# Kernel tuning notes

Measured on AMD Instinct MI355X. Metric: run time of the kernel, lower is better.

## Reference

```python
import jax, jax.numpy as jnp
import numpy as np

B, S, DIM = 2, 2048, 2048
NH, NKV = 16, 8
HD = DIM // NH  # 128
ROPE_THETA = 10000.0


def setup_inputs() -> dict:
    key = jax.random.key(0)
    ks = jax.random.split(key, 7)
    std = DIM ** -0.5
    x = jax.random.normal(ks[0], (B, S, DIM), jnp.float32)
    wq = jax.random.normal(ks[1], (NH * HD, DIM), jnp.float32) * std
    wk = jax.random.normal(ks[2], (NKV * HD, DIM), jnp.float32) * std
    wv = jax.random.normal(ks[3], (NKV * HD, DIM), jnp.float32) * std
    wo = jax.random.normal(ks[4], (DIM, NH * HD), jnp.float32) * std
    inv_freq = 1.0 / (ROPE_THETA ** (jnp.arange(0, HD, 2, dtype=jnp.float32) / HD))
    ang = jnp.arange(S, dtype=jnp.float32)[:, None] * inv_freq[None, :]  # [S, HD//2]
    freqs_cos = jnp.cos(ang)
    freqs_sin = jnp.sin(ang)
    # diffusion-style random per-batch token mask: t ~ U[0,1) per batch row
    t = jax.random.uniform(ks[5], (B, 1))
    mask = jax.random.uniform(ks[6], (B, S)) < t  # True = masked key
    mask = mask.at[:, 0].set(False)  # first token never masked
    return dict(x=x, wq=wq, wk=wk, wv=wv, wo=wo,
                freqs_cos=freqs_cos, freqs_sin=freqs_sin, mask=mask)


def _rope(x, cos, sin):
    # x: [b, s, h, d]; pairs (x[2i], x[2i+1]) rotated by angle[s, i]
    xr, xi = x[..., 0::2], x[..., 1::2]
    c = cos[None, :, None, :]
    s = sin[None, :, None, :]
    out = jnp.stack([xr * c - xi * s, xr * s + xi * c], axis=-1)
    return out.reshape(x.shape)


def reference(x, wq, wk, wv, wo, freqs_cos, freqs_sin, mask):
    b, s, _ = x.shape
    xq = jnp.einsum('bsd,ed->bse', x, wq).reshape(b, s, NH, HD)
    xk = jnp.einsum('bsd,ed->bse', x, wk).reshape(b, s, NKV, HD)
    xv = jnp.einsum('bsd,ed->bse', x, wv).reshape(b, s, NKV, HD)
    xq = _rope(xq, freqs_cos, freqs_sin)
    xk = _rope(xk, freqs_cos, freqs_sin)
    n_rep = NH // NKV
    xk = jnp.repeat(xk, n_rep, axis=2)  # repeat_kv (GQA)
    xv = jnp.repeat(xv, n_rep, axis=2)
    q = xq.transpose(0, 2, 1, 3)  # [b, h, s, d]
    k = xk.transpose(0, 2, 1, 3)
    v = xv.transpose(0, 2, 1, 3)
    scale = 1.0 / np.sqrt(HD).astype(np.float32)
    scores = jnp.einsum('bhqd,bhkd->bhqk', q, k) * scale  # [b, h, s, s]
    scores = jnp.where(mask[:, None, None, :], -jnp.inf, scores)
    probs = jax.nn.softmax(scores, axis=-1)
    out = jnp.einsum('bhqk,bhkd->bhqd', probs, v)
    out = out.transpose(0, 2, 1, 3).reshape(b, s, NH * HD)
    return jnp.einsum('bse,de->bsd', out, wo)
```

## Files before the change

kernel.cpp:

```cpp
#include <hip/hip_runtime.h>
#include <hip/hip_bf16.h>
#include <cstdint>
#include <cstddef>

#define S_LEN   2048
#define NHQ     16
#define NKV_H   8
#define HD_DIM  128
#define DMODEL  2048
#define BATCH   2
#define KVD     (NKV_H * HD_DIM)
#define QKV_LD  4096

typedef float f32x4  __attribute__((ext_vector_type(4)));
typedef __bf16 bf16x8 __attribute__((ext_vector_type(8)));
typedef __bf16 bf16x4 __attribute__((ext_vector_type(4)));
typedef short  s16x4  __attribute__((ext_vector_type(4)));

__device__ __forceinline__ void gload_lds16(const __bf16* g, __bf16* l) {
    __builtin_amdgcn_global_load_lds(
        (const __attribute__((address_space(1))) void*)g,
        (__attribute__((address_space(3))) void*)l, 16, 0, 0);
}

__global__ __launch_bounds__(256)
void prep_kernel(const unsigned* __restrict__ x, int* __restrict__ flag_x,
                 const unsigned* __restrict__ fc, int* __restrict__ flag_fc,
                 const unsigned char* __restrict__ mraw,
                 unsigned char* __restrict__ mout, int n) {
    if (blockIdx.x == 0) {
        __shared__ int cnt;
        if (threadIdx.x == 0) cnt = 0;
        __syncthreads();
        int c = 0;
        for (int j = threadIdx.x; j < 1024; j += 256) {
            unsigned hw = x[j] & 0xFFFFu;
            unsigned e  = (hw >> 7) & 0xFF;
            if (hw == 0u || (e >= 118 && e <= 132)) c++;
        }
        atomicAdd(&cnt, c);
        __syncthreads();
        if (threadIdx.x == 0) *flag_x = (cnt > 512) ? 1 : 0;
    } else if (blockIdx.x == 1) {
        if (threadIdx.x == 0) *flag_fc = (fc[0] == 0x3F803F80u) ? 1 : 0;
    } else {
        __shared__ int f_bf16, f_f32, f_u8;
        if (threadIdx.x == 0) { f_bf16 = 0; f_f32 = 0; f_u8 = 0; }
        __syncthreads();
        const unsigned* dw = (const unsigned*)mraw;
        int ndw = n / 4;
        for (int j = threadIdx.x; j < ndw; j += blockDim.x) {
            unsigned v = dw[j];
            if (v == 0x00003F80u || v == 0x3F803F80u) f_bf16 = 1;
            else if (v == 0x3F800000u) f_f32 = 1;
            else if (v & 0xFFFFFFFEu) f_u8 = 1;
        }
        __syncthreads();
        int layout;
        if (f_bf16) layout = 3;
        else if (f_f32) layout = 2;
        else if (f_u8) layout = 0;
        else layout = 1;
        for (int i = threadIdx.x; i < n; i += blockDim.x) {
            unsigned v;
            if (layout == 0)      v = mraw[i];
            else if (layout == 3) v = ((const unsigned short*)mraw)[i];
            else                  v = ((const unsigned*)mraw)[i];
            mout[i] = v ? 1u : 0u;
        }
    }
}

__device__ __forceinline__ void conv8(const void* src, __bf16* dst,
                                      size_t off, int isbf16) {
    if (isbf16) {
        *reinterpret_cast<uint4*>(dst + off) =
            *reinterpret_cast<const uint4*>((const __bf16*)src + off);
    } else {
        const float* f = (const float*)src + off;
        float4 a = *reinterpret_cast<const float4*>(f);
        float4 b = *reinterpret_cast<const float4*>(f + 4);
        bf16x8 v;
        v[0] = (__bf16)a.x; v[1] = (__bf16)a.y; v[2] = (__bf16)a.z; v[3] = (__bf16)a.w;
        v[4] = (__bf16)b.x; v[5] = (__bf16)b.y; v[6] = (__bf16)b.z; v[7] = (__bf16)b.w;
        *reinterpret_cast<bf16x8*>(dst + off) = v;
    }
}

__global__ __launch_bounds__(256)
void conv_all_kernel(const void* __restrict__ x,  const void* __restrict__ wq,
                     const void* __restrict__ wk, const void* __restrict__ wv,
                     __bf16* __restrict__ xb, __bf16* __restrict__ wcomb,
                     const int* __restrict__ dflag) {
    int i = blockIdx.x * 256 + threadIdx.x;
    int isb = *dflag;
    if (i < 1048576) {
        conv8(x, xb, (size_t)i * 8, isb);
    } else if (i < 1572864) {
        conv8(wq, wcomb, (size_t)(i - 1048576) * 8, isb);
    } else if (i < 1835008) {
        conv8(wk, wcomb + (size_t)2048 * 2048, (size_t)(i - 1572864) * 8, isb);
    } else {
        conv8(wv, wcomb + (size_t)3072 * 2048, (size_t)(i - 1835008) * 8, isb);
    }
}

__global__ __launch_bounds__(256)
void conv_bf16_strided_kernel(const void* __restrict__ src,
                              __bf16* __restrict__ dstbase,
                              int n8, const int* __restrict__ dflag) {
    int i = blockIdx.x * blockDim.x + threadIdx.x;
    if (i >= n8) return;
    size_t off = (size_t)i * 8;
    size_t row = off >> 11;
    size_t col = off & 2047;
    __bf16* dst = dstbase + row * QKV_LD + col;
    if (*dflag) {
        *reinterpret_cast<uint4*>(dst) =
            *reinterpret_cast<const uint4*>((const __bf16*)src + off);
    } else {
        const float* f = (const float*)src + off;
        float4 a = *reinterpret_cast<const float4*>(f);
        float4 b = *reinterpret_cast<const float4*>(f + 4);
        bf16x8 v;
        v[0] = (__bf16)a.x; v[1] = (__bf16)a.y; v[2] = (__bf16)a.z; v[3] = (__bf16)a.w;
        v[4] = (__bf16)b.x; v[5] = (__bf16)b.y; v[6] = (__bf16)b.z; v[7] = (__bf16)b.w;
        *reinterpret_cast<bf16x8*>(dst) = v;
    }
}

template <bool OUT_BF16>
__global__ __launch_bounds__(256)
void gemm_bt_async(const __bf16* __restrict__ A, const __bf16* __restrict__ Bw,
                   void* __restrict__ Cv, int K, int lda, int ldb, int ldc) {
    __shared__ __align__(16) __bf16 As[128 * 64];
    __shared__ __align__(16) __bf16 Bs[128 * 64];

    const int t    = threadIdx.x;
    const int w    = t >> 6;
    const int lane = t & 63;
    const int quad = lane >> 4;
    const int l16  = lane & 15;
    const int wm   = (w >> 1) * 64;
    const int wn   = (w & 1) * 64;

    const int nwg  = gridDim.x * gridDim.y;
    const int lin  = blockIdx.y * gridDim.x + blockIdx.x;
    const int swz  = (lin & 7) * (nwg >> 3) + (lin >> 3);
    const int m0   = (swz % gridDim.x) * 128;
    const int n0   = (swz / gridDim.x) * 128;

    const int rl   = lane >> 3;
    const int gl   = lane & 7;

    f32x4 acc[4][4];
#pragma unroll
    for (int i = 0; i < 4; ++i)
#pragma unroll
        for (int j = 0; j < 4; ++j) acc[i][j] = (f32x4){0.f, 0.f, 0.f, 0.f};

    for (int k0 = 0; k0 < K; k0 += 64) {
        __syncthreads();
#pragma unroll
        for (int p = 0; p < 4; ++p) {
            const int rowb = w * 32 + p * 8;
            const int r    = rowb + rl;
            const int gA   = gl ^ rl;
            gload_lds16(A  + (size_t)(m0 + r) * lda + k0 + gA * 8, &As[rowb * 64]);
            gload_lds16(Bw + (size_t)(n0 + r) * ldb + k0 + gA * 8, &Bs[rowb * 64]);
        }
        __syncthreads();
#pragma unroll
        for (int ks = 0; ks < 2; ++ks) {
            const int G = ks * 4 + quad;
            const int gsw = (G ^ (l16 & 7)) * 8;
            bf16x8 af[4], bf[4];
#pragma unroll
            for (int i = 0; i < 4; ++i)
                af[i] = *reinterpret_cast<const bf16x8*>(
                    &As[(wm + i * 16 + l16) * 64 + gsw]);
#pragma unroll
            for (int j = 0; j < 4; ++j)
                bf[j] = *reinterpret_cast<const bf16x8*>(
                    &Bs[(wn + j * 16 + l16) * 64 + gsw]);
#pragma unroll
            for (int i = 0; i < 4; ++i)
#pragma unroll
                for (int j = 0; j < 4; ++j)
                    acc[i][j] = __builtin_amdgcn_mfma_f32_16x16x32_bf16(
                        af[i], bf[j], acc[i][j], 0, 0, 0);
        }
    }
#pragma unroll
    for (int i = 0; i < 4; ++i)
#pragma unroll
        for (int r = 0; r < 4; ++r) {
            size_t m = (size_t)(m0 + wm + i * 16 + quad * 4 + r);
#pragma unroll
            for (int j = 0; j < 4; ++j) {
                int n = n0 + wn + j * 16 + l16;
                if constexpr (OUT_BF16)
                    ((__hip_bfloat16*)Cv)[m * ldc + n] = __float2bfloat16(acc[i][j][r]);
                else
                    ((float*)Cv)[m * ldc + n] = acc[i][j][r];
            }
        }
}

__global__ void rope_kernel(__hip_bfloat16* __restrict__ xqk,
                            const void* __restrict__ cosv,
                            const void* __restrict__ sinv,
                            const int* __restrict__ dflag_fc,
                            int npairs) {
    int idx = blockIdx.x * blockDim.x + threadIdx.x;
    if (idx >= npairs) return;
    int i  = idx & 63;
    int h  = (idx >> 6) % 24;
    int bs = idx / (64 * 24);
    int s  = bs & (S_LEN - 1);
    float c, sn;
    if (*dflag_fc) {
        c  = __bfloat162float(((const __hip_bfloat16*)cosv)[s * 64 + i]);
        sn = __bfloat162float(((const __hip_bfloat16*)sinv)[s * 64 + i]);
    } else {
        c  = ((const float*)cosv)[s * 64 + i];
        sn = ((const float*)sinv)[s * 64 + i];
    }
    unsigned* p = (unsigned*)(xqk + (size_t)bs * QKV_LD + h * HD_DIM) + i;
    unsigned u = *p;
    float xr = __uint_as_float(u << 16);
    float xi = __uint_as_float(u & 0xFFFF0000u);
    float o0 = xr * c - xi * sn;
    float o1 = xr * sn + xi * c;
    union { __hip_bfloat16 h2[2]; unsigned u32; } out;
    out.h2[0] = __float2bfloat16(o0);
    out.h2[1] = __float2bfloat16(o1);
    *p = out.u32;
}

__global__ __launch_bounds__(256)
void transpose_v_kernel(const __hip_bfloat16* __restrict__ xv,
                        __hip_bfloat16* __restrict__ vt) {
    __shared__ unsigned short T[32][36];
    const int t  = threadIdx.x;
    const int s0 = blockIdx.x * 32;
    const int d0 = blockIdx.y * 32;
    const int z  = blockIdx.z;
    const int b  = z >> 3;
    const int kv = z & 7;
    {
        int sr = t >> 3, dc = (t & 7) * 4;
        const unsigned short* p = (const unsigned short*)xv
            + (size_t)(b * S_LEN + s0 + sr) * QKV_LD + kv * 128 + d0 + dc;
        uint2 v = *reinterpret_cast<const uint2*>(p);
        T[sr][dc + 0] = (unsigned short)(v.x & 0xFFFFu);
        T[sr][dc + 1] = (unsigned short)(v.x >> 16);
        T[sr][dc + 2] = (unsigned short)(v.y & 0xFFFFu);
        T[sr][dc + 3] = (unsigned short)(v.y >> 16);
    }
    __syncthreads();
    {
        int dr = t >> 3, sc = (t & 7) * 4;
        unsigned w0 = (unsigned)T[sc + 0][dr] | ((unsigned)T[sc + 1][dr] << 16);
        unsigned w1 = (unsigned)T[sc + 2][dr] | ((unsigned)T[sc + 3][dr] << 16);
        unsigned short* q = (unsigned short*)vt
            + ((size_t)z * 128 + d0 + dr) * S_LEN + s0 + sc;
        uint2 v; v.x = w0; v.y = w1;
        *reinterpret_cast<uint2*>(q) = v;
    }
}

__global__ __launch_bounds__(256)
void attn_mfma2_kernel(__hip_bfloat16* qkv,
                       const __hip_bfloat16* __restrict__ vt_g,
                       const unsigned char* __restrict__ msk) {
    __shared__ __align__(16) __bf16 Ks[2][64 * 128];
    __shared__ __align__(16) __bf16 Vt[2][128 * 64];

    const int t    = threadIdx.x;
    const int w    = t >> 6;
    const int lane = t & 63;
    const int quad = lane >> 4;
    const int l16  = lane & 15;

    const int bid = ((blockIdx.x & 7) << 7) | (blockIdx.x >> 3);
    const int qt  = bid & 31;
    const int h   = (bid >> 5) & (NHQ - 1);
    const int b   = bid >> 9;
    const int kvh = h >> 1;
    const int q0  = qt * 64;

    bf16x8 qf[4];
    {
        const __bf16* qrow = (const __bf16*)qkv
            + (size_t)(b * S_LEN + q0 + w * 16 + l16) * QKV_LD + h * 128 + quad * 8;
#pragma unroll
        for (int ks = 0; ks < 4; ++ks)
            qf[ks] = *reinterpret_cast<const bf16x8*>(qrow + ks * 32);
    }

    float m_r = -INFINITY, l_r = 0.f;
    f32x4 o[8];
#pragma unroll
    for (int d0 = 0; d0 < 8; ++d0) o[d0] = (f32x4){0.f, 0.f, 0.f, 0.f};

    const float scale2 = 0.08838834764831845f * 1.4426950408889634f;
    const int gbase = lane & 48;

    const __bf16* kp[4];
    const __bf16* vp[4];
    {
        const __bf16* xk = (const __bf16*)qkv + 2048;
        const int krl = lane >> 4, kgl = lane & 15;
        const int vrl = lane >> 3, vgl = lane & 7;
#pragma unroll
        for (int p = 0; p < 4; ++p) {
            const int row = w * 16 + p * 4 + krl;
            kp[p] = xk + (size_t)(b * S_LEN + row) * QKV_LD
                       + kvh * 128 + (kgl ^ (row & 7)) * 8;
        }
#pragma unroll
        for (int p = 0; p < 4; ++p) {
            const int row = w * 32 + p * 8 + vrl;
            vp[p] = (const __bf16*)vt_g
                  + ((size_t)(b * NKV_H + kvh) * 128 + row) * S_LEN
                  + (vgl ^ (row & 7)) * 8;
        }
    }
    const unsigned char* mbase = msk + b * S_LEN;

    auto stage = [&](int sb) {
#pragma unroll
        for (int p = 0; p < 4; ++p) {
            gload_lds16(kp[p], &Ks[sb][(w * 16 + p * 4) * 128]);
            kp[p] += 64 * QKV_LD;
        }
#pragma unroll
        for (int p = 0; p < 4; ++p) {
            gload_lds16(vp[p], &Vt[sb][(w * 32 + p * 8) * 64]);
            vp[p] += 64;
        }
    };

    auto tile_body = [&](int kmask, int cb, int sb, bool do_stage) {
        if (do_stage) stage(sb);

        unsigned mk4[4];
        {
            const unsigned* mp = (const unsigned*)(mbase + kmask);
#pragma unroll
            for (int n0 = 0; n0 < 4; ++n0) mk4[n0] = mp[n0 * 4 + quad];
        }

        f32x4 sc4[4];
#pragma unroll
        for (int n0 = 0; n0 < 4; ++n0) sc4[n0] = (f32x4){0.f, 0.f, 0.f, 0.f};
        __builtin_amdgcn_s_setprio(1);
#pragma unroll
        for (int ks = 0; ks < 4; ++ks) {
            const int G = ks * 4 + quad;
#pragma unroll
            for (int n0 = 0; n0 < 4; ++n0) {
                const int row  = n0 * 16 + l16;
                const int slot = G ^ (row & 7);
                bf16x8 kf = *reinterpret_cast<const bf16x8*>(&Ks[cb][row * 128 + slot * 8]);
                sc4[n0] = __builtin_amdgcn_mfma_f32_16x16x32_bf16(kf, qf[ks], sc4[n0], 0, 0, 0);
            }
        }
        __builtin_amdgcn_s_setprio(0);

#pragma unroll
        for (int n0 = 0; n0 < 4; ++n0)
#pragma unroll
            for (int r = 0; r < 4; ++r)
                sc4[n0][r] = ((mk4[n0] >> (r * 8)) & 0xFF) ? -INFINITY : sc4[n0][r];

        float tq[4];
#pragma unroll
        for (int n0 = 0; n0 < 4; ++n0)
            tq[n0] = fmaxf(fmaxf(sc4[n0][0], sc4[n0][1]),
                           fmaxf(sc4[n0][2], sc4[n0][3]));
        float rm = fmaxf(fmaxf(tq[0], tq[1]), fmaxf(tq[2], tq[3]));
        rm = fmaxf(rm, __shfl_xor(rm, 16, 64));
        rm = fmaxf(rm, __shfl_xor(rm, 32, 64));

        bool need = (rm - m_r) * scale2 > 8.0f;
        if (__any((int)need)) {
            float mn = fmaxf(m_r, rm);
            float al = exp2f((m_r - mn) * scale2);
            m_r = mn;
            l_r *= al;
            float alq[4];
#pragma unroll
            for (int r = 0; r < 4; ++r)
                alq[r] = __shfl(al, gbase | (quad * 4 + r), 64);
#pragma unroll
            for (int d0 = 0; d0 < 8; ++d0)
#pragma unroll
                for (int r = 0; r < 4; ++r) o[d0][r] *= alq[r];
        }

        s16x4 pa[4];
        float negm = -m_r * scale2;
#pragma unroll
        for (int n0 = 0; n0 < 4; ++n0) {
            bf16x4 pk;
#pragma unroll
            for (int r = 0; r < 4; ++r) {
                float p = exp2f(fmaf(sc4[n0][r], scale2, negm));
                l_r += p;
                pk[r] = (__bf16)p;
            }
            pa[n0] = *reinterpret_cast<s16x4*>(&pk);
        }

        __builtin_amdgcn_s_setprio(1);
#pragma unroll
        for (int n0 = 0; n0 < 4; ++n0) {
            const int j    = n0 * 16 + quad * 4;
            const int gran = j >> 3;
            const int hb   = (j & 7) * 2;
#pragma unroll
            for (int d0 = 0; d0 < 8; ++d0) {
                const int row  = d0 * 16 + l16;
                const int slot = gran ^ (row & 7);
                s16x4 vb = *reinterpret_cast<const s16x4*>(
                    (const char*)(&Vt[cb][row * 64]) + slot * 16 + hb);
                o[d0] = __builtin_amdgcn_mfma_f32_16x16x16bf16_1k(
                    pa[n0], vb, o[d0], 0, 0, 0);
            }
        }
        __builtin_amdgcn_s_setprio(0);

        __syncthreads();
    };

    stage(0);
    __syncthreads();

    for (int k0 = 0; k0 < S_LEN; k0 += 128) {
        tile_body(k0,      0, 1, true);
        tile_body(k0 + 64, 1, 0, k0 + 128 < S_LEN);
    }

    float ls = l_r;
    ls += __shfl_xor(ls, 16, 64);
    ls += __shfl_xor(ls, 32, 64);
    float invl = 1.f / ls;
    float invq[4];
#pragma unroll
    for (int r = 0; r < 4; ++r)
        invq[r] = __shfl(invl, gbase | (quad * 4 + r), 64);
    __hip_bfloat16* att = qkv;
#pragma unroll
    for (int d0 = 0; d0 < 8; ++d0)
#pragma unroll
        for (int r = 0; r < 4; ++r) {
            size_t row = (size_t)(b * S_LEN + q0 + w * 16 + quad * 4 + r);
            att[row * QKV_LD + h * 128 + d0 * 16 + l16] =
                __float2bfloat16(o[d0][r] * invq[r]);
        }
}

extern "C" void kernel_launch(void* const* d_in, const int* in_sizes, int n_in,
                              void* d_out, int out_size, void* d_ws, size_t ws_size,
                              hipStream_t stream) {
    const void* x  = d_in[0];
    const void* wq = d_in[1];
    const void* wk = d_in[2];
    const void* wv = d_in[3];
    const void* wo = d_in[4];
    const void* fc = d_in[5];
    const void* fs = d_in[6];
    const unsigned char* mraw = (const unsigned char*)d_in[7];

    const int M = BATCH * S_LEN;
    char* wsb = (char*)d_ws;
    int* dflag_x  = (int*)wsb;
    int* dflag_fc = (int*)(wsb + 64);
    unsigned char* mnorm = (unsigned char*)(wsb + 128);
    __hip_bfloat16* qkv = (__hip_bfloat16*)(wsb + 8192);

    char* dob = (char*)d_out;
    __bf16* xb    = (__bf16*)dob;
    __bf16* wcomb = (__bf16*)(dob + (16u << 20));
    __hip_bfloat16* vt = (__hip_bfloat16*)d_out;

    hipLaunchKernelGGL(prep_kernel, dim3(3), dim3(256), 0, stream,
                       (const unsigned*)x, dflag_x, (const unsigned*)fc, dflag_fc,
                       mraw, mnorm, BATCH * S_LEN);

    hipLaunchKernelGGL(conv_all_kernel, dim3(8192), dim3(256), 0, stream,
                       x, wq, wk, wv, xb, wcomb, dflag_x);

    hipLaunchKernelGGL((gemm_bt_async<true>), dim3(M / 128, QKV_LD / 128), dim3(256), 0, stream,
                       xb, wcomb, (void*)qkv, DMODEL, DMODEL, DMODEL, QKV_LD);

    int npairs = M * 24 * (HD_DIM / 2);
    hipLaunchKernelGGL(rope_kernel, dim3(npairs / 256), dim3(256), 0, stream,
                       qkv, fc, fs, dflag_fc, npairs);

    hipLaunchKernelGGL(transpose_v_kernel, dim3(S_LEN / 32, HD_DIM / 32, BATCH * NKV_H),
                       dim3(256), 0, stream, qkv + 3072, vt);

    hipLaunchKernelGGL(attn_mfma2_kernel, dim3(BATCH * NHQ * (S_LEN / 64)), dim3(256), 0, stream,
                       qkv, vt, mnorm);

    hipLaunchKernelGGL(conv_bf16_strided_kernel, dim3((DMODEL * DMODEL / 8) / 256), dim3(256), 0, stream,
                       wo, (__bf16*)qkv + 2048, DMODEL * DMODEL / 8, dflag_x);

    hipLaunchKernelGGL((gemm_bt_async<false>), dim3(M / 128, DMODEL / 128), dim3(256), 0, stream,
                       (const __bf16*)qkv, (const __bf16*)qkv + 2048, d_out,
                       DMODEL, QKV_LD, QKV_LD, DMODEL);
}
```

Before: 441.4 us.

## Software-pipeline attention: overlap next tile QK^T with current softmax/PV

Restructures the attention main loop so K and V tiles are staged at different times: the QK^T MFMA for tile i+1 is issued before the softmax and PV for tile i, keeping the matrix cores busy while exp and reduction run. P is also written to a per-wave LDS buffer and reread as bf16x8 so PV uses the 16x16x32 MFMA instead of 16x16x16. This adds LDS traffic for P and raises register pressure from two live score sets, which could lower occupancy.

```diff
diff --git a/kernel.cpp b/kernel.cpp
--- a/kernel.cpp
+++ b/kernel.cpp
@@ -15,7 +15,6 @@
 typedef float f32x4  __attribute__((ext_vector_type(4)));
 typedef __bf16 bf16x8 __attribute__((ext_vector_type(8)));
 typedef __bf16 bf16x4 __attribute__((ext_vector_type(4)));
-typedef short  s16x4  __attribute__((ext_vector_type(4)));
 
 __device__ __forceinline__ void gload_lds16(const __bf16* g, __bf16* l) {
     __builtin_amdgcn_global_load_lds(
@@ -276,6 +275,7 @@
                        const unsigned char* __restrict__ msk) {
     __shared__ __align__(16) __bf16 Ks[2][64 * 128];
     __shared__ __align__(16) __bf16 Vt[2][128 * 64];
+    __shared__ __align__(16) __bf16 Ps[4][16][64];
 
     const int t    = threadIdx.x;
     const int w    = t >> 6;
@@ -329,119 +329,116 @@
     }
     const unsigned char* mbase = msk + b * S_LEN;
 
-    auto stage = [&](int sb) {
-#pragma unroll
-        for (int p = 0; p < 4; ++p) {
-            gload_lds16(kp[p], &Ks[sb][(w * 16 + p * 4) * 128]);
-            kp[p] += 64 * QKV_LD;
-        }
-#pragma unroll
-        for (int p = 0; p < 4; ++p) {
-            gload_lds16(vp[p], &Vt[sb][(w * 32 + p * 8) * 64]);
-            vp[p] += 64;
-        }
-    };
-
-    auto tile_body = [&](int kmask, int cb, int sb, bool do_stage) {
-        if (do_stage) stage(sb);
-
-        unsigned mk4[4];
-        {
-            const unsigned* mp = (const unsigned*)(mbase + kmask);
-#pragma unroll
-            for (int n0 = 0; n0 < 4; ++n0) mk4[n0] = mp[n0 * 4 + quad];
-        }
-
-        f32x4 sc4[4];
-#pragma unroll
-        for (int n0 = 0; n0 < 4; ++n0) sc4[n0] = (f32x4){0.f, 0.f, 0.f, 0.f};
-        __builtin_amdgcn_s_setprio(1);
-#pragma unroll
-        for (int ks = 0; ks < 4; ++ks) {
-            const int G = ks * 4 + quad;
-#pragma unroll
-            for (int n0 = 0; n0 < 4; ++n0) {
-                const int row  = n0 * 16 + l16;
-                const int slot = G ^ (row & 7);
-                bf16x8 kf = *reinterpret_cast<const bf16x8*>(&Ks[cb][row * 128 + slot * 8]);
-                sc4[n0] = __builtin_amdgcn_mfma_f32_16x16x32_bf16(kf, qf[ks], sc4[n0], 0, 0, 0);
-            }
-        }
-        __builtin_amdgcn_s_setprio(0);
-
-#pragma unroll
-        for (int n0 = 0; n0 < 4; ++n0)
-#pragma unroll
-            for (int r = 0; r < 4; ++r)
-                sc4[n0][r] = ((mk4[n0] >> (r * 8)) & 0xFF) ? -INFINITY : sc4[n0][r];
-
-        float tq[4];
-#pragma unroll
-        for (int n0 = 0; n0 < 4; ++n0)
-            tq[n0] = fmaxf(fmaxf(sc4[n0][0], sc4[n0][1]),
-                           fmaxf(sc4[n0][2], sc4[n0][3]));
-        float rm = fmaxf(fmaxf(tq[0], tq[1]), fmaxf(tq[2], tq[3]));
-        rm = fmaxf(rm, __shfl_xor(rm, 16, 64));
-        rm = fmaxf(rm, __shfl_xor(rm, 32, 64));
-
-        bool need = (rm - m_r) * scale2 > 8.0f;
-        if (__any((int)need)) {
-            float mn = fmaxf(m_r, rm);
-            float al = exp2f((m_r - mn) * scale2);
-            m_r = mn;
-            l_r *= al;
-            float alq[4];
-#pragma unroll
-            for (int r = 0; r < 4; ++r)
-                alq[r] = __shfl(al, gbase | (quad * 4 + r), 64);
-#pragma unroll
-            for (int d0 = 0; d0 < 8; ++d0)
-#pragma unroll
-                for (int r = 0; r < 4; ++r) o[d0][r] *= alq[r];
-        }
-
-        s16x4 pa[4];
-        float negm = -m_r * scale2;
-#pragma unroll
-        for (int n0 = 0; n0 < 4; ++n0) {
-            bf16x4 pk;
-#pragma unroll
-            for (int r = 0; r < 4; ++r) {
-                float p = exp2f(fmaf(sc4[n0][r], scale2, negm));
-                l_r += p;
-                pk[r] = (__bf16)p;
-            }
-            pa[n0] = *reinterpret_cast<s16x4*>(&pk);
-        }
-
-        __builtin_amdgcn_s_setprio(1);
-#pragma unroll
-        for (int n0 = 0; n0 < 4; ++n0) {
-            const int j    = n0 * 16 + quad * 4;
-            const int gran = j >> 3;
-            const int hb   = (j & 7) * 2;
-#pragma unroll
-            for (int d0 = 0; d0 < 8; ++d0) {
-                const int row  = d0 * 16 + l16;
-                const int slot = gran ^ (row & 7);
-                s16x4 vb = *reinterpret_cast<const s16x4*>(
-                    (const char*)(&Vt[cb][row * 64]) + slot * 16 + hb);
-                o[d0] = __builtin_amdgcn_mfma_f32_16x16x16bf16_1k(
-                    pa[n0], vb, o[d0], 0, 0, 0);
-            }
-        }
-        __builtin_amdgcn_s_setprio(0);
-
-        __syncthreads();
-    };
-
-    stage(0);
+    f32x4 scA[4], scB[4];
+    unsigned mkA[4], mkB[4];
+
+#define STAGE_K(SB) { _Pragma("unroll") \
+    for (int p_ = 0; p_ < 4; ++p_) { \
+        gload_lds16(kp[p_], &Ks[SB][(w * 16 + p_ * 4) * 128]); \
+        kp[p_] += 64 * QKV_LD; } }
+
+#define STAGE_V(SB) { _Pragma("unroll") \
+    for (int p_ = 0; p_ < 4; ++p_) { \
+        gload_lds16(vp[p_], &Vt[SB][(w * 32 + p_ * 8) * 64]); \
+        vp[p_] += 64; } }
+
+#define LOAD_MK(MK, K0) { \
+    const unsigned* mp_ = (const unsigned*)(mbase + (K0)); \
+    _Pragma("unroll") for (int n_ = 0; n_ < 4; ++n_) MK[n_] = mp_[n_ * 4 + quad]; }
+
+#define QKT(CB, SC) { \
+    _Pragma("unroll") for (int n_ = 0; n_ < 4; ++n_) SC[n_] = (f32x4){0.f, 0.f, 0.f, 0.f}; \
+    _Pragma("unroll") for (int ks_ = 0; ks_ < 4; ++ks_) { \
+        const int G_ = ks_ * 4 + quad; \
+        _Pragma("unroll") for (int n_ = 0; n_ < 4; ++n_) { \
+            const int row_  = n_ * 16 + l16; \
+            const int slot_ = G_ ^ (row_ & 7); \
+            bf16x8 kf_ = *reinterpret_cast<const bf16x8*>(&Ks[CB][row_ * 128 + slot_ * 8]); \
+            SC[n_] = __builtin_amdgcn_mfma_f32_16x16x32_bf16(kf_, qf[ks_], SC[n_], 0, 0, 0); } } }
+
+#define SMPV(SC, MK, CB) { \
+    _Pragma("unroll") for (int n_ = 0; n_ < 4; ++n_) \
+        _Pragma("unroll") for (int r_ = 0; r_ < 4; ++r_) \
+            SC[n_][r_] = ((MK[n_] >> (r_ * 8)) & 0xFF) ? -INFINITY : SC[n_][r_]; \
+    float tq_[4]; \
+    _Pragma("unroll") for (int n_ = 0; n_ < 4; ++n_) \
+        tq_[n_] = fmaxf(fmaxf(SC[n_][0], SC[n_][1]), fmaxf(SC[n_][2], SC[n_][3])); \
+    float rm_ = fmaxf(fmaxf(tq_[0], tq_[1]), fmaxf(tq_[2], tq_[3])); \
+    rm_ = fmaxf(rm_, __shfl_xor(rm_, 16, 64)); \
+    rm_ = fmaxf(rm_, __shfl_xor(rm_, 32, 64)); \
+    bool need_ = (rm_ - m_r) * scale2 > 8.0f; \
+    if (__any((int)need_)) { \
+        float mn_ = fmaxf(m_r, rm_); \
+        float al_ = exp2f((m_r - mn_) * scale2); \
+        m_r = mn_; l_r *= al_; \
+        float alq_[4]; \
+        _Pragma("unroll") for (int r_ = 0; r_ < 4; ++r_) \
+            alq_[r_] = __shfl(al_, gbase | (quad * 4 + r_), 64); \
+        _Pragma("unroll") for (int d_ = 0; d_ < 8; ++d_) \
+            _Pragma("unroll") for (int r_ = 0; r_ < 4; ++r_) o[d_][r_] *= alq_[r_]; } \
+    float negm_ = -m_r * scale2; \
+    _Pragma("unroll") for (int n_ = 0; n_ < 4; ++n_) { \
+        _Pragma("unroll") for (int r_ = 0; r_ < 4; ++r_) { \
+            float p_ = exp2f(fmaf(SC[n_][r_], scale2, negm_)); \
+            SC[n_][r_] = p_; l_r += p_; } \
+        const int kb_    = n_ * 16 + quad * 4; \
+        const int gran_  = kb_ >> 3; \
+        const int half4_ = kb_ & 4; \
+        const int slot_  = gran_ ^ (l16 & 7); \
+        bf16x4 pk_; \
+        pk_[0] = (__bf16)SC[n_][0]; pk_[1] = (__bf16)SC[n_][1]; \
+        pk_[2] = (__bf16)SC[n_][2]; pk_[3] = (__bf16)SC[n_][3]; \
+        *reinterpret_cast<bf16x4*>(&Ps[w][l16][slot_ * 8 + half4_]) = pk_; } \
+    __builtin_amdgcn_s_setprio(1); \
+    _Pragma("unroll") for (int kk_ = 0; kk_ < 64; kk_ += 32) { \
+        const int Gp_    = (kk_ >> 3) + quad; \
+        const int slotp_ = Gp_ ^ (l16 & 7); \
+        bf16x8 af_ = *reinterpret_cast<const bf16x8*>(&Ps[w][l16][slotp_ * 8]); \
+        _Pragma("unroll") for (int d_ = 0; d_ < 8; ++d_) { \
+            const int row_  = d_ * 16 + l16; \
+            const int slot_ = Gp_ ^ (row_ & 7); \
+            bf16x8 bf_ = *reinterpret_cast<const bf16x8*>(&Vt[CB][row_ * 64 + slot_ * 8]); \
+            o[d_] = __builtin_amdgcn_mfma_f32_16x16x32_bf16(af_, bf_, o[d_], 0, 0, 0); } } \
+    __builtin_amdgcn_s_setprio(0); }
+
+    STAGE_K(0);
     __syncthreads();
 
-    for (int k0 = 0; k0 < S_LEN; k0 += 128) {
-        tile_body(k0,      0, 1, true);
-        tile_body(k0 + 64, 1, 0, k0 + 128 < S_LEN);
-    }
+    STAGE_K(1);
+    STAGE_V(0);
+    LOAD_MK(mkA, 0);
+    QKT(0, scA);
+    __syncthreads();
+
+    for (int it = 0; it < 15; ++it) {
+        const int k0 = it * 128 + 64;
+        STAGE_K(0);
+        STAGE_V(1);
+        LOAD_MK(mkB, k0);
+        QKT(1, scB);
+        SMPV(scA, mkA, 0);
+        __syncthreads();
+        STAGE_K(1);
+        STAGE_V(0);
+        LOAD_MK(mkA, k0 + 64);
+        QKT(0, scA);
+        SMPV(scB, mkB, 1);
+        __syncthreads();
+    }
+
+    STAGE_V(1);
+    LOAD_MK(mkB, 1984);
+    QKT(1, scB);
+    SMPV(scA, mkA, 0);
+    __syncthreads();
+
+    SMPV(scB, mkB, 1);
+
+#undef STAGE_K
+#undef STAGE_V
+#undef LOAD_MK
+#undef QKT
+#undef SMPV
 
     float ls = l_r;
     ls += __shfl_xor(ls, 16, 64);
```

New measurement: 426.8 us. -3.3%, faster.
